# Performance work log

Hardware: AMD Instinct MI355X
Metric: run time of the kernel (lower is better)

## Reference

```python
import jax, jax.numpy as jnp
import numpy as np

DIM = 1024
HEADS = 16
HEAD_DIM = DIM // HEADS
T_MAX = 128
V = 12
T = 128
B = 4
N = V * T + 1  # 1537, includes cls token


def setup_inputs() -> dict:
    key = jax.random.key(0)
    ks = jax.random.split(key, 9)
    s = 0.02
    return {
        "x": jax.random.normal(ks[0], (B, N, DIM), dtype=jnp.float32),
        "qkv_w": jax.random.normal(ks[1], (3 * DIM, DIM), dtype=jnp.float32) * s,
        "in_proj_w": jax.random.normal(ks[2], (3 * DIM, DIM), dtype=jnp.float32) * s,
        "in_proj_b": jax.random.normal(ks[3], (3 * DIM,), dtype=jnp.float32) * s,
        "out_proj_w": jax.random.normal(ks[4], (DIM, DIM), dtype=jnp.float32) * s,
        "out_proj_b": jax.random.normal(ks[5], (DIM,), dtype=jnp.float32) * s,
        "proj_w": jax.random.normal(ks[6], (DIM, DIM), dtype=jnp.float32) * s,
        "proj_b": jax.random.normal(ks[7], (DIM,), dtype=jnp.float32) * s,
        "ids_restore": jax.random.randint(ks[8], (B, V * T), 0, 1000000, dtype=jnp.int64),
        "V_input": V,
        "T_input": T,
    }


def _rope_tables(dtype):
    # theta_d = 10000^{-2d/head_dim}, positions 0..T_max (position 0 is the cls slot)
    theta = 10000.0 ** (-jnp.arange(0, HEAD_DIM, 2, dtype=dtype) / HEAD_DIM)  # (hd/2,)
    pos = jnp.arange(1 + T_MAX, dtype=dtype)
    ang = pos[:, None] * theta[None, :]  # (1+T_max, hd/2)
    return jnp.cos(ang), jnp.sin(ang)


def _rotate(t, cos_g, sin_g):
    # t: (B, N, D); cos_g/sin_g: (B, N-1, 1, hd/2) gathered per non-cls token
    b, n, d = t.shape
    t4 = t.reshape(b, n, HEADS, HEAD_DIM)
    re, im = t4[..., ::2], t4[..., 1::2]  # even/odd interleave -> (B,N,H,hd/2)
    # cls token uses position 0: cos=1, sin=0 -> identity rotation, halves concatenated
    cls = jnp.concatenate([re[:, :1], im[:, :1]], axis=-1)  # (B,1,H,hd)
    rest = jnp.concatenate(
        [re[:, 1:] * cos_g - im[:, 1:] * sin_g,
         re[:, 1:] * sin_g + im[:, 1:] * cos_g], axis=-1)  # (B,N-1,H,hd)
    return jnp.concatenate([cls, rest], axis=1).reshape(b, n, d)


def reference(x, qkv_w, in_proj_w, in_proj_b, out_proj_w, out_proj_b,
              proj_w, proj_b, ids_restore, V_input, T_input):
    b, n, d = x.shape
    # --- qkv projection (no bias) ---
    qkv = jnp.einsum('bnd,ed->bne', x, qkv_w)  # (B,N,3D)
    q, k, v = jnp.split(qkv, 3, axis=-1)
    # --- temporal RoPE with ids_restore-based gather ---
    cos_t, sin_t = _rope_tables(x.dtype)  # (1+T_max, hd/2)
    ids_shuffle = jnp.argsort(ids_restore, axis=1)[:, : n - 1] % V_input  # (B,N-1)
    cos_g = cos_t[ids_shuffle + 1][:, :, None, :]  # gather from cos[:,1:] slice
    sin_g = sin_t[ids_shuffle + 1][:, :, None, :]
    q = _rotate(q, cos_g, sin_g)
    k = _rotate(k, cos_g, sin_g)
    # --- nn.MultiheadAttention (batch_first, no mask, eval) ---
    wq, wk, wv = in_proj_w[:d], in_proj_w[d:2 * d], in_proj_w[2 * d:]
    bq, bk, bv = in_proj_b[:d], in_proj_b[d:2 * d], in_proj_b[2 * d:]
    qp = (jnp.einsum('bnd,ed->bne', q, wq) + bq).reshape(b, n, HEADS, HEAD_DIM)
    kp = (jnp.einsum('bnd,ed->bne', k, wk) + bk).reshape(b, n, HEADS, HEAD_DIM)
    vp = (jnp.einsum('bnd,ed->bne', v, wv) + bv).reshape(b, n, HEADS, HEAD_DIM)
    scale = 1.0 / jnp.sqrt(jnp.asarray(HEAD_DIM, x.dtype))
    scores = jnp.einsum('bqhe,bkhe->bhqk', qp * scale, kp)  # (B,H,N,N)
    attn = jax.nn.softmax(scores, axis=-1)
    ctx = jnp.einsum('bhqk,bkhe->bqhe', attn, vp).reshape(b, n, d)
    mha_out = jnp.einsum('bnd,ed->bne', ctx, out_proj_w) + out_proj_b
    # --- final projection ---
    out = jnp.einsum('bnd,ed->bne', mha_out, proj_w) + proj_b
    return out


if __name__ == '__main__':
    inp = setup_inputs()
    print(reference(**inp).shape)
```

## Files before the change

kernel.cpp:

```cpp
#include <hip/hip_runtime.h>
#include <math.h>

#define B_ 4
#define NTOK 1537
#define NH 16
#define NROWS 6148
#define RPAD 6272
#define KDIM 1024
#define NKT 49

typedef __attribute__((ext_vector_type(8))) short short8;
typedef __attribute__((ext_vector_type(4))) float f32x4;
typedef __attribute__((ext_vector_type(16))) float f32x16;
typedef __attribute__((ext_vector_type(4))) unsigned short ushort4v;
typedef __attribute__((ext_vector_type(4))) unsigned int uint4v;
typedef __attribute__((ext_vector_type(2))) unsigned int uint2v;

__device__ __forceinline__ float bf2f(unsigned short u){
  unsigned int x = ((unsigned int)u) << 16;
  return __uint_as_float(x);
}
__device__ __forceinline__ unsigned short f2bf(float f){
  unsigned int x = __float_as_uint(f);
  x += 0x7fff + ((x >> 16) & 1);
  return (unsigned short)(x >> 16);
}
__device__ __forceinline__ unsigned int pack_bf16(float lo, float hi){
  return (unsigned int)f2bf(lo) | ((unsigned int)f2bf(hi) << 16);
}
__device__ __forceinline__ unsigned int pack_bf16_fast(float lo, float hi){
  unsigned int ue = __float_as_uint(lo) + 0x8000u;
  unsigned int uo = __float_as_uint(hi) + 0x8000u;
  return __builtin_amdgcn_perm(uo, ue, 0x07060302u);
}
__device__ __forceinline__ float fast_exp2(float x){
  return __builtin_amdgcn_exp2f(x);
}
__device__ __forceinline__ uint2v permswap(unsigned int a, unsigned int b){
  return __builtin_amdgcn_permlane32_swap(a, b, false, false);
}
__device__ __forceinline__ void gload_lds16(const void* g, void* l){
  __builtin_amdgcn_global_load_lds((const __attribute__((address_space(1))) unsigned int*)g,
                                   (__attribute__((address_space(3))) unsigned int*)l, 16, 0, 0);
}
__device__ __forceinline__ f32x4 mfma16(short8 a, short8 b, f32x4 c){
  return __builtin_amdgcn_mfma_f32_16x16x32_bf16(a, b, c, 0, 0, 0);
}
__device__ __forceinline__ f32x16 mfma32(short8 a, short8 b, f32x16 c){
  return __builtin_amdgcn_mfma_f32_32x32x16_bf16(a, b, c, 0, 0, 0);
}

__global__ __launch_bounds__(256) void cvt_w_kernel(const float* __restrict__ src,
                                                    unsigned short* __restrict__ dst, int n){
  int i = (blockIdx.x*256 + threadIdx.x)*4;
  if (i >= n) return;
  f32x4 v = *(const f32x4*)(src + i);
  ushort4v o;
  #pragma unroll
  for (int j=0;j<4;j++) o[j] = f2bf(v[j]);
  *(ushort4v*)(dst + i) = o;
}

__global__ __launch_bounds__(256) void cvt_x_kernel(const float* __restrict__ x,
                                                    unsigned short* __restrict__ xb){
  size_t i = ((size_t)blockIdx.x*256 + threadIdx.x)*4;
  if (i >= (size_t)RPAD*KDIM) return;
  size_t row = i >> 10;
  ushort4v o;
  if (row < NROWS){
    f32x4 v = *(const f32x4*)(x + i);
    #pragma unroll
    for (int j=0;j<4;j++) o[j] = f2bf(v[j]);
  } else {
    o = (ushort4v)0;
  }
  *(ushort4v*)(xb + i) = o;
}

__global__ void rope_tables_kernel(float* __restrict__ ct, float* __restrict__ st){
  int i = threadIdx.x;
  if (i >= 13*32) return;
  int p = i >> 5, j = i & 31;
  float th = powf(10000.f, -(float)j * (1.f/32.f));
  float ang = (float)p * th;
  ct[i] = cosf(ang);
  st[i] = sinf(ang);
}

__global__ __launch_bounds__(256) void argsort_kernel(const int* __restrict__ ids,
                                                      int* __restrict__ postab){
  __shared__ int vals[1536];
  int b = blockIdx.x;
  const int* src = ids + b*1536;
  for (int i=threadIdx.x; i<1536; i+=256) vals[i] = src[i];
  __syncthreads();
  int i = blockIdx.y*256 + threadIdx.x;
  int v = vals[i];
  int rank = 0;
  for (int j=0;j<1536;j++){
    int u = vals[j];
    rank += (u < v) || (u == v && j < i);
  }
  postab[b*1536 + rank] = (i % 12) + 1;
}

__global__ __launch_bounds__(256) void rope_kernel(unsigned short* __restrict__ qkv,
                                                   const int* __restrict__ postab,
                                                   const float* __restrict__ ct,
                                                   const float* __restrict__ st){
  int idx = blockIdx.x*256 + threadIdx.x;
  if (idx >= B_*NTOK*NH) return;
  int h = idx & 15;
  int bn = idx >> 4;
  int b = bn / NTOK;
  int n = bn - b*NTOK;
  unsigned short* rowp = qkv + (size_t)bn*3072;
  int pos = (n == 0) ? 0 : postab[b*1536 + (n-1)];
  const float* cr = ct + pos*32;
  const float* sr = st + pos*32;
  #pragma unroll
  for (int part=0; part<2; part++){
    unsigned short* p = rowp + part*1024 + h*64;
    uint4v vv[8];
    #pragma unroll
    for (int i=0;i<8;i++) vv[i] = ((const uint4v*)p)[i];
    unsigned short* tp = (unsigned short*)vv;
    unsigned short ov[64];
    if (n == 0){
      #pragma unroll
      for (int j=0;j<32;j++){ ov[j] = tp[2*j]; ov[32+j] = tp[2*j+1]; }
    } else {
      #pragma unroll
      for (int j=0;j<32;j++){
        float re = bf2f(tp[2*j]), im = bf2f(tp[2*j+1]);
        float c = cr[j], s = sr[j];
        ov[j]    = f2bf(re*c - im*s);
        ov[32+j] = f2bf(re*s + im*c);
      }
    }
    #pragma unroll
    for (int i=0;i<8;i++) ((uint4v*)p)[i] = ((const uint4v*)ov)[i];
  }
}

__device__ __forceinline__ void gemm_body(const unsigned short* __restrict__ A, int lda,
    const unsigned short* __restrict__ W,
    const float* __restrict__ bias, float scale,
    unsigned short* __restrict__ outb, float* __restrict__ outf, int ldo, int mvalid,
    int rowBase, int colBase)
{
  __shared__ alignas(16) unsigned short At[128][32];
  __shared__ alignas(16) unsigned short Bt[128][32];
  int t = threadIdx.x, w = t >> 6, lane = t & 63;
  int g = lane >> 4, l15 = lane & 15;
  int rb = (w >> 1) * 64, cb = (w & 1) * 64;
  f32x4 acc[4][4];
  #pragma unroll
  for (int m=0;m<4;m++)
    #pragma unroll
    for (int n=0;n<4;n++) acc[m][n] = 0.f;
  int srow = lane >> 2;
  int scol = (lane & 3) * 8;
  for (int kb = 0; kb < KDIM; kb += 32){
    __syncthreads();
    #pragma unroll
    for (int i=0;i<2;i++){
      int rr = i*64 + w*16 + srow;
      gload_lds16(A + (size_t)(rowBase + rr)*lda + kb + scol, &At[i*64 + w*16][0]);
      gload_lds16(W + (size_t)(colBase + rr)*KDIM + kb + scol, &Bt[i*64 + w*16][0]);
    }
    __syncthreads();
    short8 af[4], bf[4];
    #pragma unroll
    for (int m=0;m<4;m++) af[m] = *(const short8*)&At[rb + m*16 + l15][g*8];
    #pragma unroll
    for (int n=0;n<4;n++) bf[n] = *(const short8*)&Bt[cb + n*16 + l15][g*8];
    #pragma unroll
    for (int m=0;m<4;m++)
      #pragma unroll
      for (int n=0;n<4;n++)
        acc[m][n] = mfma16(af[m], bf[n], acc[m][n]);
  }
  #pragma unroll
  for (int m=0;m<4;m++)
    #pragma unroll
    for (int n=0;n<4;n++){
      int col = colBase + cb + n*16 + l15;
      float bv = bias ? bias[col] : 0.f;
      #pragma unroll
      for (int r=0;r<4;r++){
        int row = rowBase + rb + m*16 + g*4 + r;
        if (row < mvalid){
          float v = (acc[m][n][r] + bv) * scale;
          if (outf) outf[(size_t)row*ldo + col] = v;
          else      outb[(size_t)row*ldo + col] = f2bf(v);
        }
      }
    }
}

__global__ __launch_bounds__(256) void gemm_kernel(const unsigned short* __restrict__ A, int lda,
    const unsigned short* __restrict__ W,
    const float* __restrict__ bias, float scale,
    unsigned short* __restrict__ outb, float* __restrict__ outf, int ldo, int mvalid)
{
  gemm_body(A, lda, W, bias, scale, outb, outf, ldo, mvalid,
            blockIdx.x*128, blockIdx.y*128);
}

__global__ __launch_bounds__(256) void gemm_inproj_kernel(const unsigned short* __restrict__ qkvb,
    const unsigned short* __restrict__ ipwb, const float* __restrict__ ipb,
    unsigned short* __restrict__ qpb, unsigned short* __restrict__ kpb,
    unsigned short* __restrict__ vpb)
{
  int z = blockIdx.z;
  const unsigned short* A = qkvb + z*1024;
  const unsigned short* W = ipwb + (size_t)z*1024*1024;
  const float* bias = ipb + z*1024;
  float scale = (z == 0) ? 0.125f*1.44269504f : 1.f;
  unsigned short* outb = (z == 0) ? qpb : (z == 1 ? kpb : vpb);
  gemm_body(A, 3072, W, bias, scale, outb, nullptr, 1024, NROWS,
            blockIdx.x*128, blockIdx.y*128);
}

__global__ __launch_bounds__(256) void kfrag_kernel(const unsigned short* __restrict__ kp,
                                                    unsigned short* __restrict__ kf){
  int bh = blockIdx.x, kt = blockIdx.y;
  int b = bh >> 4, h = bh & 15;
  int t = threadIdx.x;
  int lane = t & 63, c = t >> 6;
  int l31 = lane & 31, hh = lane >> 5;
  int key = kt*32 + l31; if (key > NTOK-1) key = NTOK-1;
  uint4v v = *(const uint4v*)(kp + (size_t)(b*NTOK + key)*KDIM + h*64 + c*16 + hh*8);
  *(uint4v*)(kf + (size_t)(bh*NKT + kt)*2048 + c*512 + lane*8) = v;
}

__global__ __launch_bounds__(256) void vfrag_kernel(const unsigned short* __restrict__ vp,
                                                    unsigned short* __restrict__ vf){
  __shared__ alignas(16) unsigned short Tl[32][72];
  int bh = blockIdx.x, kt = blockIdx.y;
  int b = bh >> 4, h = bh & 15;
  int t = threadIdx.x;
  {
    int r = t >> 3, ch = t & 7;
    int key = kt*32 + r;
    uint4v v;
    if (key < NTOK){
      v = *(const uint4v*)(vp + (size_t)(b*NTOK + key)*KDIM + h*64 + ch*8);
    } else v = (uint4v)0;
    *(uint4v*)&Tl[r][ch*8] = v;
  }
  __syncthreads();
  {
    int lane = t & 63, w = t >> 6;
    int l31 = lane & 31, hh = lane >> 5;
    int dblk = w >> 1, c = w & 1;
    unsigned short ov[8];
    #pragma unroll
    for (int j=0;j<8;j++) ov[j] = Tl[c*16 + hh*8 + j][dblk*32 + l31];
    *(uint4v*)(vf + (size_t)(bh*NKT + kt)*2048 + w*512 + lane*8) = *(const uint4v*)ov;
  }
}

__global__ __launch_bounds__(256) void attn_kernel(const unsigned short* __restrict__ qp,
    const unsigned short* __restrict__ kf, const unsigned short* __restrict__ vf,
    unsigned short* __restrict__ ctx)
{
  int bh = blockIdx.x;
  int qt = blockIdx.y;
  int b = bh >> 4, hd = bh & 15;
  int t = threadIdx.x, w = t >> 6, lane = t & 63;
  int l31 = lane & 31, hh = lane >> 5;
  int qrow = qt*128 + w*32 + l31;
  int qcl = qrow > NTOK-1 ? NTOK-1 : qrow;
  const unsigned short* qb = qp + (((size_t)(b*NTOK + qcl)*NH + hd) << 6) + hh*8;
  short8 qf[4];
  #pragma unroll
  for (int c=0;c<4;c++) qf[c] = *(const short8*)(qb + c*16);
  const unsigned short* kfb = kf + (size_t)(bh*NKT)*2048 + lane*8;
  const unsigned short* vfb = vf + (size_t)(bh*NKT)*2048 + lane*8;
  float m_ = -3e38f, l_ = 0.f;
  f32x16 o0 = 0.f, o1 = 0.f;

  auto soft_pv = [&](f32x16 cc, short8 va00, short8 va01, short8 va10, short8 va11){
    float t0 = fmaxf(fmaxf(cc[0],cc[1]), fmaxf(cc[2],cc[3]));
    float t1 = fmaxf(fmaxf(cc[4],cc[5]), fmaxf(cc[6],cc[7]));
    float t2 = fmaxf(fmaxf(cc[8],cc[9]), fmaxf(cc[10],cc[11]));
    float t3 = fmaxf(fmaxf(cc[12],cc[13]), fmaxf(cc[14],cc[15]));
    float mx = fmaxf(fmaxf(t0,t1), fmaxf(t2,t3));
    {
      uint2v pr = permswap(__float_as_uint(mx), __float_as_uint(mx));
      mx = fmaxf(__uint_as_float(pr[0]), __uint_as_float(pr[1]));
    }
    if (!__all(mx <= m_ + 11.5f)){
      float mn = fmaxf(m_, mx);
      float al = fast_exp2(m_ - mn);
      m_ = mn;
      l_ *= al;
      #pragma unroll
      for (int i=0;i<16;i++){ o0[i] *= al; o1[i] *= al; }
    }
    float p[16], rs = 0.f;
    #pragma unroll
    for (int i=0;i<16;i++){ p[i] = fast_exp2(cc[i] - m_); }
    #pragma unroll
    for (int i=0;i<16;i++) rs += p[i];
    l_ += rs;
    unsigned int W[8];
    #pragma unroll
    for (int wd=0; wd<8; wd++) W[wd] = pack_bf16_fast(p[2*wd], p[2*wd+1]);
    uint2v e0 = permswap(W[0], W[2]);
    uint2v e1 = permswap(W[1], W[3]);
    uint2v e2 = permswap(W[4], W[6]);
    uint2v e3 = permswap(W[5], W[7]);
    uint4v u0, u1;
    u0[0]=e0[0]; u0[1]=e1[0]; u0[2]=e0[1]; u0[3]=e1[1];
    u1[0]=e2[0]; u1[1]=e3[0]; u1[2]=e2[1]; u1[3]=e3[1];
    short8 pb0, pb1;
    __builtin_memcpy(&pb0, &u0, 16);
    __builtin_memcpy(&pb1, &u1, 16);
    o0 = mfma32(va00, pb0, o0);
    o0 = mfma32(va01, pb1, o0);
    o1 = mfma32(va10, pb0, o1);
    o1 = mfma32(va11, pb1, o1);
  };

  short8 ka[4];
  #pragma unroll
  for (int c=0;c<4;c++) ka[c] = *(const short8*)(kfb + c*512);
  f32x16 cc = 0.f;
  cc = mfma32(ka[0], qf[0], cc);
  cc = mfma32(ka[1], qf[1], cc);
  cc = mfma32(ka[2], qf[2], cc);
  cc = mfma32(ka[3], qf[3], cc);
  #pragma unroll
  for (int c=0;c<4;c++) ka[c] = *(const short8*)(kfb + 2048 + c*512);

  for (int kt=0; kt<48; ++kt){
    const unsigned short* vB = vfb + (size_t)kt*2048;
    short8 va00 = *(const short8*)(vB);
    short8 va01 = *(const short8*)(vB + 512);
    short8 va10 = *(const short8*)(vB + 1024);
    short8 va11 = *(const short8*)(vB + 1536);
    f32x16 cn = 0.f;
    cn = mfma32(ka[0], qf[0], cn);
    cn = mfma32(ka[1], qf[1], cn);
    cn = mfma32(ka[2], qf[2], cn);
    cn = mfma32(ka[3], qf[3], cn);
    int ktn = kt+2 < NKT-1 ? kt+2 : NKT-1;
    const unsigned short* kB = kfb + (size_t)ktn*2048;
    #pragma unroll
    for (int c=0;c<4;c++) ka[c] = *(const short8*)(kB + c*512);
    soft_pv(cc, va00, va01, va10, va11);
    cc = cn;
  }
  {
    const unsigned short* vB = vfb + (size_t)48*2048;
    short8 va00 = *(const short8*)(vB);
    short8 va01 = *(const short8*)(vB + 512);
    short8 va10 = *(const short8*)(vB + 1024);
    short8 va11 = *(const short8*)(vB + 1536);
    #pragma unroll
    for (int i=0;i<16;i++) cc[i] = (i == 0 && hh == 0) ? cc[i] : -1e30f;
    soft_pv(cc, va00, va01, va10, va11);
  }
  {
    uint2v pr = permswap(__float_as_uint(l_), __float_as_uint(l_));
    l_ = __uint_as_float(pr[0]) + __uint_as_float(pr[1]);
  }
  if (qrow < NTOK){
    float inv = 1.f / l_;
    unsigned short* cb = ctx + (((size_t)(b*NTOK + qrow)*NH + hd) << 6) + 4*hh;
    #pragma unroll
    for (int s=0;s<4;s++){
      uint2v u;
      u[0] = pack_bf16(o0[4*s]*inv,   o0[4*s+1]*inv);
      u[1] = pack_bf16(o0[4*s+2]*inv, o0[4*s+3]*inv);
      *(uint2v*)(cb + 8*s) = u;
    }
    #pragma unroll
    for (int s=0;s<4;s++){
      uint2v u;
      u[0] = pack_bf16(o1[4*s]*inv,   o1[4*s+1]*inv);
      u[1] = pack_bf16(o1[4*s+2]*inv, o1[4*s+3]*inv);
      *(uint2v*)(cb + 32 + 8*s) = u;
    }
  }
}

extern "C" void kernel_launch(void* const* d_in, const int* in_sizes, int n_in,
                              void* d_out, int out_size, void* d_ws, size_t ws_size,
                              hipStream_t stream)
{
  const float* x    = (const float*)d_in[0];
  const float* qkvw = (const float*)d_in[1];
  const float* ipw  = (const float*)d_in[2];
  const float* ipb  = (const float*)d_in[3];
  const float* opw  = (const float*)d_in[4];
  const float* opb  = (const float*)d_in[5];
  const float* pw   = (const float*)d_in[6];
  const float* pb   = (const float*)d_in[7];
  const int*   ids  = (const int*)d_in[8];
  float* out = (float*)d_out;

  char* p = (char*)d_ws;
  auto alloc = [&](size_t bytes)->char* {
    char* r = p; p += (bytes + 255) & ~(size_t)255; return r;
  };
  unsigned short* xb    = (unsigned short*)alloc((size_t)RPAD*1024*2);
  unsigned short* qkvwb = (unsigned short*)alloc((size_t)3072*1024*2);
  unsigned short* ipwb  = (unsigned short*)alloc((size_t)3072*1024*2);
  unsigned short* opwb  = (unsigned short*)alloc((size_t)1024*1024*2);
  unsigned short* pwb   = (unsigned short*)alloc((size_t)1024*1024*2);
  unsigned short* qkvb  = (unsigned short*)alloc((size_t)RPAD*3072*2);
  unsigned short* qpb   = (unsigned short*)alloc((size_t)RPAD*1024*2);
  unsigned short* kpb   = (unsigned short*)alloc((size_t)RPAD*1024*2);
  unsigned short* vpb   = (unsigned short*)alloc((size_t)RPAD*1024*2);
  unsigned short* ctxb  = (unsigned short*)alloc((size_t)RPAD*1024*2);
  unsigned short* mhab  = (unsigned short*)alloc((size_t)RPAD*1024*2);
  int*   postab = (int*)alloc((size_t)B_*1536*4);
  float* ctab   = (float*)alloc(13*32*4);
  float* stab   = (float*)alloc(13*32*4);
  unsigned short* vfb = xb;
  unsigned short* kfb = qkvb;

  cvt_w_kernel<<<3072, 256, 0, stream>>>(qkvw, qkvwb, 3072*1024);
  cvt_w_kernel<<<3072, 256, 0, stream>>>(ipw,  ipwb,  3072*1024);
  cvt_w_kernel<<<1024, 256, 0, stream>>>(opw,  opwb,  1024*1024);
  cvt_w_kernel<<<1024, 256, 0, stream>>>(pw,   pwb,   1024*1024);
  cvt_x_kernel<<<RPAD, 256, 0, stream>>>(x, xb);
  rope_tables_kernel<<<1, 512, 0, stream>>>(ctab, stab);
  argsort_kernel<<<dim3(B_, 6), 256, 0, stream>>>(ids, postab);

  gemm_kernel<<<dim3(RPAD/128, 3072/128), 256, 0, stream>>>(xb, 1024, qkvwb, nullptr, 1.f,
                                                            qkvb, nullptr, 3072, NROWS);
  rope_kernel<<<(B_*NTOK*NH + 255)/256, 256, 0, stream>>>(qkvb, postab, ctab, stab);
  gemm_inproj_kernel<<<dim3(RPAD/128, 8, 3), 256, 0, stream>>>(qkvb, ipwb, ipb, qpb, kpb, vpb);
  kfrag_kernel<<<dim3(B_*NH, NKT), 256, 0, stream>>>(kpb, kfb);
  vfrag_kernel<<<dim3(B_*NH, NKT), 256, 0, stream>>>(vpb, vfb);
  attn_kernel<<<dim3(B_*NH, 13), 256, 0, stream>>>(qpb, kfb, vfb, ctxb);
  gemm_kernel<<<dim3(RPAD/128, 8), 256, 0, stream>>>(ctxb, 1024, opwb, opb, 1.f,
                                                     mhab, nullptr, 1024, NROWS);
  gemm_kernel<<<dim3(RPAD/128, 8), 256, 0, stream>>>(mhab, 1024, pwb,  pb,  1.f,
                                                     nullptr, out, 1024, NROWS);
}
```

Baseline: 390.2 us.

## Fold out-proj into final proj and V weights into a single precomputed matrix

Pre-multiplies weight matrices on the device so that two activation GEMMs disappear. The out_proj and proj weights are combined into one 1024x1024 matrix with a fused bias, and the v-slice of qkv_w is folded into the in_proj V weight, so V comes straight from x. Two small 1024^3 weight GEMMs, transpose-convert kernels and a bias GEMV are added, and the qkv buffer shrinks to the q and k parts. Rounding the fused weights to bf16 changes numerics slightly.

```diff
diff --git a/kernel.cpp b/kernel.cpp
--- a/kernel.cpp
+++ b/kernel.cpp
@@ -59,6 +59,29 @@
   #pragma unroll
   for (int j=0;j<4;j++) o[j] = f2bf(v[j]);
   *(ushort4v*)(dst + i) = o;
+}
+
+__global__ __launch_bounds__(256) void cvt_wT_kernel(const float* __restrict__ src, int r0,
+                                                     unsigned short* __restrict__ dst){
+  __shared__ float Tl[64][65];
+  int ct = blockIdx.x, rt = blockIdx.y;
+  int t = threadIdx.x;
+  int i = t >> 4, j4 = (t & 15) * 4;
+  #pragma unroll
+  for (int s = 0; s < 4; s++){
+    int rl = s*16 + i;
+    f32x4 v = *(const f32x4*)(src + (size_t)(r0 + rt*64 + rl)*1024 + ct*64 + j4);
+    Tl[rl][j4+0]=v[0]; Tl[rl][j4+1]=v[1]; Tl[rl][j4+2]=v[2]; Tl[rl][j4+3]=v[3];
+  }
+  __syncthreads();
+  #pragma unroll
+  for (int s = 0; s < 4; s++){
+    int cl = s*16 + i;
+    ushort4v o;
+    #pragma unroll
+    for (int k=0;k<4;k++) o[k] = f2bf(Tl[j4+k][cl]);
+    *(ushort4v*)(dst + (size_t)(ct*64 + cl)*1024 + rt*64 + j4) = o;
+  }
 }
 
 __global__ __launch_bounds__(256) void cvt_x_kernel(const float* __restrict__ x,
@@ -75,6 +98,15 @@
     o = (ushort4v)0;
   }
   *(ushort4v*)(xb + i) = o;
+}
+
+__global__ __launch_bounds__(256) void fuse_bias_kernel(const float* __restrict__ pw,
+    const float* __restrict__ opb, const float* __restrict__ pb, float* __restrict__ bf){
+  int c = blockIdx.x*256 + threadIdx.x;
+  const float* row = pw + (size_t)c*1024;
+  float s = 0.f;
+  for (int e=0; e<1024; e++) s += row[e]*opb[e];
+  bf[c] = s + pb[c];
 }
 
 __global__ void rope_tables_kernel(float* __restrict__ ct, float* __restrict__ st){
@@ -114,7 +146,7 @@
   int bn = idx >> 4;
   int b = bn / NTOK;
   int n = bn - b*NTOK;
-  unsigned short* rowp = qkv + (size_t)bn*3072;
+  unsigned short* rowp = qkv + (size_t)bn*2048;
   int pos = (n == 0) ? 0 : postab[b*1536 + (n-1)];
   const float* cr = ct + pos*32;
   const float* sr = st + pos*32;
@@ -208,18 +240,30 @@
             blockIdx.x*128, blockIdx.y*128);
 }
 
-__global__ __launch_bounds__(256) void gemm_inproj_kernel(const unsigned short* __restrict__ qkvb,
+__global__ __launch_bounds__(256) void gemm_inproj_kernel(const unsigned short* __restrict__ qkb,
     const unsigned short* __restrict__ ipwb, const float* __restrict__ ipb,
-    unsigned short* __restrict__ qpb, unsigned short* __restrict__ kpb,
-    unsigned short* __restrict__ vpb)
+    unsigned short* __restrict__ qpb, unsigned short* __restrict__ kpb)
 {
   int z = blockIdx.z;
-  const unsigned short* A = qkvb + z*1024;
+  const unsigned short* A = qkb + z*1024;
   const unsigned short* W = ipwb + (size_t)z*1024*1024;
   const float* bias = ipb + z*1024;
   float scale = (z == 0) ? 0.125f*1.44269504f : 1.f;
-  unsigned short* outb = (z == 0) ? qpb : (z == 1 ? kpb : vpb);
-  gemm_body(A, 3072, W, bias, scale, outb, nullptr, 1024, NROWS,
+  unsigned short* outb = (z == 0) ? qpb : kpb;
+  gemm_body(A, 2048, W, bias, scale, outb, nullptr, 1024, NROWS,
+            blockIdx.x*128, blockIdx.y*128);
+}
+
+__global__ __launch_bounds__(256) void gemm_prep_kernel(const unsigned short* __restrict__ pwb,
+    const unsigned short* __restrict__ opwT, const unsigned short* __restrict__ wv,
+    const unsigned short* __restrict__ qkvwTv,
+    unsigned short* __restrict__ Wfb, unsigned short* __restrict__ Wvb)
+{
+  int z = blockIdx.z;
+  const unsigned short* A = z ? wv : pwb;
+  const unsigned short* W = z ? qkvwTv : opwT;
+  unsigned short* outb = z ? Wvb : Wfb;
+  gemm_body(A, 1024, W, nullptr, 1.f, outb, nullptr, 1024, 1024,
             blockIdx.x*128, blockIdx.y*128);
 }
 
@@ -407,40 +451,48 @@
   auto alloc = [&](size_t bytes)->char* {
     char* r = p; p += (bytes + 255) & ~(size_t)255; return r;
   };
-  unsigned short* xb    = (unsigned short*)alloc((size_t)RPAD*1024*2);
-  unsigned short* qkvwb = (unsigned short*)alloc((size_t)3072*1024*2);
-  unsigned short* ipwb  = (unsigned short*)alloc((size_t)3072*1024*2);
-  unsigned short* opwb  = (unsigned short*)alloc((size_t)1024*1024*2);
-  unsigned short* pwb   = (unsigned short*)alloc((size_t)1024*1024*2);
-  unsigned short* qkvb  = (unsigned short*)alloc((size_t)RPAD*3072*2);
-  unsigned short* qpb   = (unsigned short*)alloc((size_t)RPAD*1024*2);
-  unsigned short* kpb   = (unsigned short*)alloc((size_t)RPAD*1024*2);
-  unsigned short* vpb   = (unsigned short*)alloc((size_t)RPAD*1024*2);
-  unsigned short* ctxb  = (unsigned short*)alloc((size_t)RPAD*1024*2);
-  unsigned short* mhab  = (unsigned short*)alloc((size_t)RPAD*1024*2);
+  unsigned short* xb     = (unsigned short*)alloc((size_t)RPAD*1024*2);
+  unsigned short* qkvwb  = (unsigned short*)alloc((size_t)2048*1024*2);
+  unsigned short* ipwb   = (unsigned short*)alloc((size_t)3072*1024*2);
+  unsigned short* pwb    = (unsigned short*)alloc((size_t)1024*1024*2);
+  unsigned short* opwT   = (unsigned short*)alloc((size_t)1024*1024*2);
+  unsigned short* qkvwTv = (unsigned short*)alloc((size_t)1024*1024*2);
+  unsigned short* Wfb    = (unsigned short*)alloc((size_t)1024*1024*2);
+  unsigned short* Wvb    = (unsigned short*)alloc((size_t)1024*1024*2);
+  float*          bfb    = (float*)alloc(1024*4);
+  unsigned short* qkb    = (unsigned short*)alloc((size_t)RPAD*2048*2);
+  unsigned short* qpb    = (unsigned short*)alloc((size_t)RPAD*1024*2);
+  unsigned short* kpb    = (unsigned short*)alloc((size_t)RPAD*1024*2);
+  unsigned short* vpb    = (unsigned short*)alloc((size_t)RPAD*1024*2);
+  unsigned short* ctxb   = (unsigned short*)alloc((size_t)RPAD*1024*2);
   int*   postab = (int*)alloc((size_t)B_*1536*4);
   float* ctab   = (float*)alloc(13*32*4);
   float* stab   = (float*)alloc(13*32*4);
   unsigned short* vfb = xb;
-  unsigned short* kfb = qkvb;
-
-  cvt_w_kernel<<<3072, 256, 0, stream>>>(qkvw, qkvwb, 3072*1024);
+  unsigned short* kfb = qkb;
+
+  cvt_w_kernel<<<2048, 256, 0, stream>>>(qkvw, qkvwb, 2048*1024);
   cvt_w_kernel<<<3072, 256, 0, stream>>>(ipw,  ipwb,  3072*1024);
-  cvt_w_kernel<<<1024, 256, 0, stream>>>(opw,  opwb,  1024*1024);
   cvt_w_kernel<<<1024, 256, 0, stream>>>(pw,   pwb,   1024*1024);
+  cvt_wT_kernel<<<dim3(16,16), 256, 0, stream>>>(opw,  0,    opwT);
+  cvt_wT_kernel<<<dim3(16,16), 256, 0, stream>>>(qkvw, 2048, qkvwTv);
   cvt_x_kernel<<<RPAD, 256, 0, stream>>>(x, xb);
   rope_tables_kernel<<<1, 512, 0, stream>>>(ctab, stab);
   argsort_kernel<<<dim3(B_, 6), 256, 0, stream>>>(ids, postab);
 
-  gemm_kernel<<<dim3(RPAD/128, 3072/128), 256, 0, stream>>>(xb, 1024, qkvwb, nullptr, 1.f,
-                                                            qkvb, nullptr, 3072, NROWS);
-  rope_kernel<<<(B_*NTOK*NH + 255)/256, 256, 0, stream>>>(qkvb, postab, ctab, stab);
-  gemm_inproj_kernel<<<dim3(RPAD/128, 8, 3), 256, 0, stream>>>(qkvb, ipwb, ipb, qpb, kpb, vpb);
+  gemm_prep_kernel<<<dim3(8, 8, 2), 256, 0, stream>>>(pwb, opwT, ipwb + (size_t)2048*1024,
+                                                      qkvwTv, Wfb, Wvb);
+  fuse_bias_kernel<<<4, 256, 0, stream>>>(pw, opb, pb, bfb);
+
+  gemm_kernel<<<dim3(RPAD/128, 16), 256, 0, stream>>>(xb, 1024, qkvwb, nullptr, 1.f,
+                                                      qkb, nullptr, 2048, NROWS);
+  rope_kernel<<<(B_*NTOK*NH + 255)/256, 256, 0, stream>>>(qkb, postab, ctab, stab);
+  gemm_inproj_kernel<<<dim3(RPAD/128, 8, 2), 256, 0, stream>>>(qkb, ipwb, ipb, qpb, kpb);
+  gemm_kernel<<<dim3(RPAD/128, 8), 256, 0, stream>>>(xb, 1024, Wvb, ipb + 2048, 1.f,
+                                                     vpb, nullptr, 1024, NROWS);
   kfrag_kernel<<<dim3(B_*NH, NKT), 256, 0, stream>>>(kpb, kfb);
   vfrag_kernel<<<dim3(B_*NH, NKT), 256, 0, stream>>>(vpb, vfb);
   attn_kernel<<<dim3(B_*NH, 13), 256, 0, stream>>>(qpb, kfb, vfb, ctxb);
-  gemm_kernel<<<dim3(RPAD/128, 8), 256, 0, stream>>>(ctxb, 1024, opwb, opb, 1.f,
-                                                     mhab, nullptr, 1024, NROWS);
-  gemm_kernel<<<dim3(RPAD/128, 8), 256, 0, stream>>>(mhab, 1024, pwb,  pb,  1.f,
+  gemm_kernel<<<dim3(RPAD/128, 8), 256, 0, stream>>>(ctxb, 1024, Wfb, bfb, 1.f,
                                                      nullptr, out, 1024, NROWS);
 }
```

Measured after the change: 424.7 us. 1.09x slower.
